# Optimization experiments

Measured on AMD Instinct MI355X. Metric: run time of the kernel, lower is better.

## Reference

```python
import jax, jax.numpy as jnp
import numpy as np

# Module constants (match init_kwargs)
H = 16            # num_heads
K = 64            # max_kernel_size
MAX_FREQ = 16.0
MIN_FREQ = 1.0
HALF_S = 16       # int(32**(1/1)) // 2
S = 2 * HALF_S + 1  # 33 sample offsets: -16..16
MAX_RECEPTIVE = HALF_S * MAX_FREQ  # 256.0


def setup_inputs() -> dict:
    key = jax.random.key(0)
    ks = jax.random.split(key, 6)
    B, L, C = 1, 4096, 1024
    x = jax.random.normal(ks[0], (B, L, C), dtype=jnp.float32)
    # Learned params (random small scale so offsets/kernels vary; torch inits
    # wave_proj to zeros but that degenerates the math under test).
    Ww = jax.random.normal(ks[1], (2 * H, C), dtype=jnp.float32) * 0.02
    bw = jnp.zeros((2 * H,), dtype=jnp.float32)
    Wk = jax.random.normal(ks[2], (H * K, C), dtype=jnp.float32) * 0.02
    bk = jnp.zeros((H * K,), dtype=jnp.float32)
    Wo = jax.random.normal(ks[3], (C, C), dtype=jnp.float32) * 0.02
    return {"x": x, "Ww": Ww, "bw": bw, "Wk": Wk, "bk": bk, "Wo": Wo}


def reference(x, Ww, bw, Wk, bk, Wo):
    B, L, C = x.shape
    D = C // H
    dt = x.dtype
    grid = jnp.arange(-HALF_S, HALF_S + 1, dtype=dt)  # (S,)

    # Predict per-position frequency / phase (averaged over heads)
    wp = jax.nn.silu(x @ Ww.T + bw).reshape(B, L, 2, H)
    freq = jax.nn.sigmoid(wp[:, :, 0]) * (MAX_FREQ - MIN_FREQ) + MIN_FREQ  # (B,L,H)
    phase = jnp.tanh(wp[:, :, 1]) * MAX_FREQ
    freq_avg = freq.mean(-1)    # (B,L)
    phase_avg = phase.mean(-1)  # (B,L)

    # Sample positions & gather indices
    rel_pos = grid[None, None, :] * freq_avg[..., None] + phase_avg[..., None]  # (B,L,S)
    centers = jnp.arange(L, dtype=dt)
    sample_pos = centers[None, :, None] + rel_pos                               # (B,L,S)
    valid = (sample_pos >= 0) & (sample_pos < L)
    sample_idx = jnp.clip(sample_pos.astype(jnp.int32), 0, L - 1)               # trunc toward 0, like torch .long()

    # Gather values: (B,L,S,C) -> (B,L,H,S,D)
    values = jax.vmap(lambda xf, idx: xf[idx])(x, sample_idx)
    values = values.reshape(B, L, S, H, D).transpose(0, 1, 3, 2, 4)

    # Kernel profile, linearly interpolated to sample positions
    kernel_max = jax.nn.silu(x @ Wk.T + bk).reshape(B, L, H, K)
    norm_pos = jnp.clip((rel_pos + MAX_RECEPTIVE) / (2.0 * MAX_RECEPTIVE), 0.0, 1.0)
    idx_float = norm_pos * (K - 1)                       # (B,L,S)
    idx_floor = jnp.clip(idx_float.astype(jnp.int32), 0, K - 2)
    w_ceil = (idx_float - idx_floor.astype(dt))[:, :, None, :]  # (B,L,1,S)
    w_floor = 1.0 - w_ceil
    ifl = jnp.broadcast_to(idx_floor[:, :, None, :], (B, L, H, S))
    k_floor = jnp.take_along_axis(kernel_max, ifl, axis=-1)
    k_ceil = jnp.take_along_axis(kernel_max, ifl + 1, axis=-1)
    kernel = (k_floor * w_floor + k_ceil * w_ceil) * valid[:, :, None, :].astype(dt)
    kernel = kernel / (kernel.sum(-1, keepdims=True) + 1e-8)

    out = jnp.einsum('blhsd,blhs->blhd', values, kernel).reshape(B, L, C)
    out = jax.nn.silu(out @ Wo.T)
    return out
```

## Files before the change

kernel.cpp:

```cpp
#include <hip/hip_runtime.h>
#include <math.h>

#define LDIM 4096
#define CDIM 1024
#define HDIM 16
#define KDIM 64
#define SDIM 33
#define HALF_SS 16
#define MAXF 16.0f
#define MINF 1.0f
#define MAXR 256.0f

typedef double d4 __attribute__((ext_vector_type(4)));

#define MFMA_F64 __builtin_amdgcn_mfma_f64_16x16x4f64

__device__ __forceinline__ float sigmoid_np(float z) {
  float e = (float)exp(-(double)z);
  return __fdiv_rn(1.0f, __fadd_rn(1.0f, e));
}
__device__ __forceinline__ float silu_f(float z) {
  return __fmul_rn(z, sigmoid_np(z));
}

__device__ __forceinline__ float np_pairwise_sum(const float* a, int n) {
  float r[8];
#pragma unroll
  for (int j = 0; j < 8; ++j) r[j] = a[j];
  int i = 8;
  for (; i + 8 <= n; i += 8)
#pragma unroll
    for (int j = 0; j < 8; ++j) r[j] = __fadd_rn(r[j], a[i + j]);
  float res = __fadd_rn(__fadd_rn(__fadd_rn(r[0], r[1]), __fadd_rn(r[2], r[3])),
                        __fadd_rn(__fadd_rn(r[4], r[5]), __fadd_rn(r[6], r[7])));
  for (; i < n; ++i) res = __fadd_rn(res, a[i]);
  return res;
}

__global__ __launch_bounds__(256) void wave_kernel(
    const float* __restrict__ x, const float* __restrict__ Ww,
    const float* __restrict__ bw, float* __restrict__ fa, float* __restrict__ pa) {
  __shared__ float xs[CDIM];
  __shared__ float wp[2 * HDIM];
  int l = blockIdx.x;
  int tid = threadIdx.x;
  const float* xrow = x + (size_t)l * CDIM;
  for (int c = tid; c < CDIM; c += 256) xs[c] = xrow[c];
  __syncthreads();
  int j = tid >> 3, sub = tid & 7;
  const float* wrow = Ww + j * CDIM;
  double acc = 0.0;
  for (int c = sub; c < CDIM; c += 8) acc += (double)xs[c] * (double)wrow[c];
  for (int off = 4; off; off >>= 1) acc += __shfl_down(acc, off, 8);
  if (sub == 0) {
    float v32 = (float)(acc + (double)bw[j]);
    wp[j] = silu_f(v32);
  }
  __syncthreads();
  if (tid == 0) {
    float fv[HDIM], pv[HDIM];
    for (int h = 0; h < HDIM; ++h) {
      fv[h] = __fadd_rn(__fmul_rn(sigmoid_np(wp[h]), MAXF - MINF), MINF);
      float t32 = (float)tanh((double)wp[HDIM + h]);
      pv[h] = __fmul_rn(t32, MAXF);
    }
    fa[l] = __fdiv_rn(np_pairwise_sum(fv, HDIM), (float)HDIM);
    pa[l] = __fdiv_rn(np_pairwise_sum(pv, HDIM), (float)HDIM);
  }
}

__global__ __launch_bounds__(256) void gemm_bt_silu_f64(
    const float* __restrict__ A, const float* __restrict__ B,
    const float* __restrict__ bias, float* __restrict__ Cout,
    int M, int N, int Kd) {
  __shared__ float Asf[128][36];
  __shared__ float Bsf[64][36];
  int tid = threadIdx.x;
  int w  = tid >> 6;
  int l  = tid & 63;
  int m0 = blockIdx.y * 128, n0 = blockIdx.x * 64;

  d4 zv = (d4)(0.0);
  double lane_d = (double)l;
  d4 pA = MFMA_F64(lane_d, 1.0, zv, 0, 0, 0);
  d4 pB = MFMA_F64(1.0, lane_d, zv, 0, 0, 0);
  int sa0 = (int)pA[0], sb0 = (int)pB[0];
  bool aH1 = ((sa0 & 3) == 0);
  bool bH1 = ((sb0 & 3) == 0);
  int lmA = aH1 ? (l & 15) : (l >> 2);
  int lqA = aH1 ? (l >> 4) : (l & 3);
  int lmB = bH1 ? (l & 15) : (l >> 2);
  int lqB = bH1 ? (l >> 4) : (l & 3);
  int di[4], dj[4];
#pragma unroll
  for (int r = 0; r < 4; ++r) {
    int va = (int)pA[r], vb = (int)pB[r];
    di[r] = (aH1 ? ((va - 96) >> 2) : ((va - 6) >> 4)) & 15;
    dj[r] = (bH1 ? ((vb - 96) >> 2) : ((vb - 6) >> 4)) & 15;
  }

  d4 acc[8];
#pragma unroll
  for (int i = 0; i < 8; ++i) acc[i] = (d4)(0.0);

  for (int kt = 0; kt < Kd; kt += 32) {
#pragma unroll
    for (int qi = 0; qi < 4; ++qi) {
      int e = tid + 256 * qi;
      int row = e >> 3, j = e & 7;
      float4 v = *(const float4*)(A + (size_t)(m0 + row) * Kd + kt + 4 * j);
      Asf[row][j] = v.x; Asf[row][j + 8] = v.y;
      Asf[row][j + 16] = v.z; Asf[row][j + 24] = v.w;
    }
#pragma unroll
    for (int qi = 0; qi < 2; ++qi) {
      int e = tid + 256 * qi;
      int row = e >> 3, j = e & 7;
      float4 v = *(const float4*)(B + (size_t)(n0 + row) * Kd + kt + 4 * j);
      Bsf[row][j] = v.x; Bsf[row][j + 8] = v.y;
      Bsf[row][j + 16] = v.z; Bsf[row][j + 24] = v.w;
    }
    __syncthreads();
#pragma unroll
    for (int t = 0; t < 2; ++t) {
      float4 bv = *(const float4*)&Bsf[16 * w + lmB][8 * lqB + 4 * t];
      float4 av0 = *(const float4*)&Asf[lmA][8 * lqA + 4 * t];
      float4 av1 = *(const float4*)&Asf[16 + lmA][8 * lqA + 4 * t];
      float4 av2 = *(const float4*)&Asf[32 + lmA][8 * lqA + 4 * t];
      float4 av3 = *(const float4*)&Asf[48 + lmA][8 * lqA + 4 * t];
      float4 av4 = *(const float4*)&Asf[64 + lmA][8 * lqA + 4 * t];
      float4 av5 = *(const float4*)&Asf[80 + lmA][8 * lqA + 4 * t];
      float4 av6 = *(const float4*)&Asf[96 + lmA][8 * lqA + 4 * t];
      float4 av7 = *(const float4*)&Asf[112 + lmA][8 * lqA + 4 * t];
      float bs[4] = {bv.x, bv.y, bv.z, bv.w};
      float as0[4] = {av0.x, av0.y, av0.z, av0.w};
      float as1[4] = {av1.x, av1.y, av1.z, av1.w};
      float as2[4] = {av2.x, av2.y, av2.z, av2.w};
      float as3[4] = {av3.x, av3.y, av3.z, av3.w};
      float as4[4] = {av4.x, av4.y, av4.z, av4.w};
      float as5[4] = {av5.x, av5.y, av5.z, av5.w};
      float as6[4] = {av6.x, av6.y, av6.z, av6.w};
      float as7[4] = {av7.x, av7.y, av7.z, av7.w};
#pragma unroll
      for (int s = 0; s < 4; ++s) {
        double bd = (double)bs[s];
        acc[0] = MFMA_F64((double)as0[s], bd, acc[0], 0, 0, 0);
        acc[1] = MFMA_F64((double)as1[s], bd, acc[1], 0, 0, 0);
        acc[2] = MFMA_F64((double)as2[s], bd, acc[2], 0, 0, 0);
        acc[3] = MFMA_F64((double)as3[s], bd, acc[3], 0, 0, 0);
        acc[4] = MFMA_F64((double)as4[s], bd, acc[4], 0, 0, 0);
        acc[5] = MFMA_F64((double)as5[s], bd, acc[5], 0, 0, 0);
        acc[6] = MFMA_F64((double)as6[s], bd, acc[6], 0, 0, 0);
        acc[7] = MFMA_F64((double)as7[s], bd, acc[7], 0, 0, 0);
      }
    }
    __syncthreads();
  }

#pragma unroll
  for (int mt = 0; mt < 8; ++mt) {
#pragma unroll
    for (int r = 0; r < 4; ++r) {
      int mm = m0 + 16 * mt + di[r];
      int nn = n0 + 16 * w + dj[r];
      float v32 = (float)acc[mt][r];
      v32 = __fadd_rn(v32, bias[nn]);
      Cout[(size_t)mm * N + nn] = silu_f(v32);
    }
  }
}

__global__ __launch_bounds__(256) void gemm_bt_silu_f32(
    const float* __restrict__ A, const float* __restrict__ B,
    float* __restrict__ Cout, int M, int N, int Kd) {
  __shared__ float Asf[16][128];
  __shared__ float Bsf[16][128];
  int tid = threadIdx.x;
  int tx = tid & 15, ty = tid >> 4;
  int m0 = blockIdx.y * 128, n0 = blockIdx.x * 128;
  float acc[8][8] = {};
  for (int kt = 0; kt < Kd; kt += 16) {
#pragma unroll
    for (int q = 0; q < 2; ++q) {
      int e = tid + 256 * q;
      int row = e >> 2, kq = (e & 3) * 4;
      float4 va = *(const float4*)(A + (size_t)(m0 + row) * Kd + kt + kq);
      Asf[kq + 0][row] = va.x; Asf[kq + 1][row] = va.y;
      Asf[kq + 2][row] = va.z; Asf[kq + 3][row] = va.w;
      float4 vb = *(const float4*)(B + (size_t)(n0 + row) * Kd + kt + kq);
      Bsf[kq + 0][row] = vb.x; Bsf[kq + 1][row] = vb.y;
      Bsf[kq + 2][row] = vb.z; Bsf[kq + 3][row] = vb.w;
    }
    __syncthreads();
#pragma unroll
    for (int kk = 0; kk < 16; ++kk) {
      float4 a0 = *(const float4*)&Asf[kk][ty * 8];
      float4 a1 = *(const float4*)&Asf[kk][ty * 8 + 4];
      float4 b0 = *(const float4*)&Bsf[kk][tx * 8];
      float4 b1 = *(const float4*)&Bsf[kk][tx * 8 + 4];
      float a[8] = {a0.x, a0.y, a0.z, a0.w, a1.x, a1.y, a1.z, a1.w};
      float b[8] = {b0.x, b0.y, b0.z, b0.w, b1.x, b1.y, b1.z, b1.w};
#pragma unroll
      for (int i = 0; i < 8; ++i)
#pragma unroll
        for (int j2 = 0; j2 < 8; ++j2) acc[i][j2] += a[i] * b[j2];
    }
    __syncthreads();
  }
#pragma unroll
  for (int i = 0; i < 8; ++i) {
    int mm = m0 + ty * 8 + i;
#pragma unroll
    for (int j2 = 0; j2 < 8; ++j2) {
      int nn = n0 + tx * 8 + j2;
      Cout[(size_t)mm * N + nn] = silu_f(acc[i][j2]);
    }
  }
}

__global__ __launch_bounds__(256) void conv_kernel(
    const float* __restrict__ x, const float* __restrict__ km,
    const float* __restrict__ fa, const float* __restrict__ pa,
    float* __restrict__ conv) {
  int l = blockIdx.x;
  int tid = threadIdx.x;
  __shared__ int s_idx[SDIM];
  __shared__ int s_ifl[SDIM];
  __shared__ float s_wc[SDIM];
  __shared__ float s_val[SDIM];
  __shared__ float kern[HDIM][SDIM];
  __shared__ float s_den[HDIM];
  if (tid < SDIM) {
    float f = fa[l], p = pa[l];
    float rel = __fadd_rn(__fmul_rn((float)(tid - HALF_SS), f), p);
    float pos = __fadd_rn((float)l, rel);
    bool valid = (pos >= 0.f) && (pos < (float)LDIM);
    int idx = (int)pos;
    idx = min(max(idx, 0), LDIM - 1);
    s_idx[tid] = idx;
    s_val[tid] = valid ? 1.f : 0.f;
    float np_ = __fdiv_rn(__fadd_rn(rel, MAXR), 2.f * MAXR);
    np_ = fminf(fmaxf(np_, 0.f), 1.f);
    float idxf = __fmul_rn(np_, (float)(KDIM - 1));
    int ifl = (int)idxf;
    ifl = min(max(ifl, 0), KDIM - 2);
    s_ifl[tid] = ifl;
    s_wc[tid] = __fsub_rn(idxf, (float)ifl);
  }
  __syncthreads();
  for (int t = tid; t < HDIM * SDIM; t += 256) {
    int h = t / SDIM, s = t - h * SDIM;
    const float* kb = km + (size_t)l * CDIM + h * KDIM;
    float wc = s_wc[s];
    float wf = __fsub_rn(1.f, wc);
    float v = __fadd_rn(__fmul_rn(kb[s_ifl[s]], wf), __fmul_rn(kb[s_ifl[s] + 1], wc));
    kern[h][s] = __fmul_rn(v, s_val[s]);
  }
  __syncthreads();
  if (tid < HDIM) {
    float sum = np_pairwise_sum(&kern[tid][0], SDIM);
    s_den[tid] = __fadd_rn(sum, 1e-8f);
  }
  __syncthreads();
  for (int t = tid; t < HDIM * SDIM; t += 256) {
    int h = t / SDIM, s = t - h * SDIM;
    kern[h][s] = __fdiv_rn(kern[h][s], s_den[h]);
  }
  __syncthreads();
  float acc[4] = {0.f, 0.f, 0.f, 0.f};
  for (int s = 0; s < SDIM; ++s) {
    const float* xr = x + (size_t)s_idx[s] * CDIM;
#pragma unroll
    for (int q = 0; q < 4; ++q) {
      int c = tid + q * 256;
      acc[q] = __fadd_rn(acc[q], __fmul_rn(xr[c], kern[c >> 6][s]));
    }
  }
#pragma unroll
  for (int q = 0; q < 4; ++q) {
    int c = tid + q * 256;
    conv[(size_t)l * CDIM + c] = acc[q];
  }
}

extern "C" void kernel_launch(void* const* d_in, const int* in_sizes, int n_in,
                              void* d_out, int out_size, void* d_ws, size_t ws_size,
                              hipStream_t stream) {
  const float* x  = (const float*)d_in[0];
  const float* Ww = (const float*)d_in[1];
  const float* bw = (const float*)d_in[2];
  const float* Wk = (const float*)d_in[3];
  const float* bk = (const float*)d_in[4];
  const float* Wo = (const float*)d_in[5];
  float* out = (float*)d_out;

  float* fa   = (float*)d_ws;
  float* pa   = fa + LDIM;
  float* km   = pa + LDIM;
  float* conv = km + (size_t)LDIM * CDIM;

  wave_kernel<<<LDIM, 256, 0, stream>>>(x, Ww, bw, fa, pa);

  dim3 kmgrid(CDIM / 64, LDIM / 128);
  gemm_bt_silu_f64<<<kmgrid, 256, 0, stream>>>(x, Wk, bk, km, LDIM, CDIM, CDIM);

  conv_kernel<<<LDIM, 256, 0, stream>>>(x, km, fa, pa, conv);

  dim3 ogrid(CDIM / 128, LDIM / 128);
  gemm_bt_silu_f32<<<ogrid, 256, 0, stream>>>(conv, Wo, out, LDIM, CDIM, CDIM);
}
```

Baseline: 456.1 us.

## Double-buffer f64 MFMA GEMM tiles and retile output GEMM to 512 threads

The f64-MFMA GEMM that produces the kernel profile now uses two shared-memory buffers, so global loads for the next K tile are issued before the current tile's MFMAs and written to the other buffer afterwards. This hides global load latency and removes one barrier per iteration, at the cost of doubled LDS and more live registers. The output GEMM moves from 256 to 512 threads, each computing a 4x8 micro-tile, with padded LDS rows and float4 stores. This trades more threads per block for fewer accumulators per thread.

```diff
diff --git a/kernel.cpp b/kernel.cpp
--- a/kernel.cpp
+++ b/kernel.cpp
@@ -73,8 +73,8 @@
     const float* __restrict__ A, const float* __restrict__ B,
     const float* __restrict__ bias, float* __restrict__ Cout,
     int M, int N, int Kd) {
-  __shared__ float Asf[128][36];
-  __shared__ float Bsf[64][36];
+  __shared__ float Asf[2][128][36];
+  __shared__ float Bsf[2][64][36];
   int tid = threadIdx.x;
   int w  = tid >> 6;
   int l  = tid & 63;
@@ -103,35 +103,59 @@
 #pragma unroll
   for (int i = 0; i < 8; ++i) acc[i] = (d4)(0.0);
 
-  for (int kt = 0; kt < Kd; kt += 32) {
-#pragma unroll
-    for (int qi = 0; qi < 4; ++qi) {
-      int e = tid + 256 * qi;
-      int row = e >> 3, j = e & 7;
-      float4 v = *(const float4*)(A + (size_t)(m0 + row) * Kd + kt + 4 * j);
-      Asf[row][j] = v.x; Asf[row][j + 8] = v.y;
-      Asf[row][j + 16] = v.z; Asf[row][j + 24] = v.w;
-    }
-#pragma unroll
-    for (int qi = 0; qi < 2; ++qi) {
-      int e = tid + 256 * qi;
-      int row = e >> 3, j = e & 7;
-      float4 v = *(const float4*)(B + (size_t)(n0 + row) * Kd + kt + 4 * j);
-      Bsf[row][j] = v.x; Bsf[row][j + 8] = v.y;
-      Bsf[row][j + 16] = v.z; Bsf[row][j + 24] = v.w;
-    }
-    __syncthreads();
+  int rA = tid >> 3, jc = tid & 7;
+  const float* Agp = A + (size_t)(m0 + rA) * Kd + 4 * jc;
+  const float* Bgp = B + (size_t)(n0 + rA) * Kd + 4 * jc;
+
+  {
+    float4 a0 = *(const float4*)(Agp);
+    float4 a1 = *(const float4*)(Agp + (size_t)32 * Kd);
+    float4 a2 = *(const float4*)(Agp + (size_t)64 * Kd);
+    float4 a3 = *(const float4*)(Agp + (size_t)96 * Kd);
+    float4 b0 = *(const float4*)(Bgp);
+    float4 b1 = *(const float4*)(Bgp + (size_t)32 * Kd);
+    Asf[0][rA +  0][jc] = a0.x; Asf[0][rA +  0][jc + 8] = a0.y;
+    Asf[0][rA +  0][jc + 16] = a0.z; Asf[0][rA +  0][jc + 24] = a0.w;
+    Asf[0][rA + 32][jc] = a1.x; Asf[0][rA + 32][jc + 8] = a1.y;
+    Asf[0][rA + 32][jc + 16] = a1.z; Asf[0][rA + 32][jc + 24] = a1.w;
+    Asf[0][rA + 64][jc] = a2.x; Asf[0][rA + 64][jc + 8] = a2.y;
+    Asf[0][rA + 64][jc + 16] = a2.z; Asf[0][rA + 64][jc + 24] = a2.w;
+    Asf[0][rA + 96][jc] = a3.x; Asf[0][rA + 96][jc + 8] = a3.y;
+    Asf[0][rA + 96][jc + 16] = a3.z; Asf[0][rA + 96][jc + 24] = a3.w;
+    Bsf[0][rA +  0][jc] = b0.x; Bsf[0][rA +  0][jc + 8] = b0.y;
+    Bsf[0][rA +  0][jc + 16] = b0.z; Bsf[0][rA +  0][jc + 24] = b0.w;
+    Bsf[0][rA + 32][jc] = b1.x; Bsf[0][rA + 32][jc + 8] = b1.y;
+    Bsf[0][rA + 32][jc + 16] = b1.z; Bsf[0][rA + 32][jc + 24] = b1.w;
+  }
+  __syncthreads();
+
+  const int NT = Kd >> 5;
+  int cur = 0;
+  for (int tt = 0; tt < NT; ++tt) {
+    float4 qa0, qa1, qa2, qa3, qb0, qb1;
+    bool pf = (tt + 1 < NT);
+    if (pf) {
+      int ko = (tt + 1) * 32;
+      qa0 = *(const float4*)(Agp + ko);
+      qa1 = *(const float4*)(Agp + (size_t)32 * Kd + ko);
+      qa2 = *(const float4*)(Agp + (size_t)64 * Kd + ko);
+      qa3 = *(const float4*)(Agp + (size_t)96 * Kd + ko);
+      qb0 = *(const float4*)(Bgp + ko);
+      qb1 = *(const float4*)(Bgp + (size_t)32 * Kd + ko);
+    }
+    const float (*As)[36] = Asf[cur];
+    const float (*Bs)[36] = Bsf[cur];
 #pragma unroll
     for (int t = 0; t < 2; ++t) {
-      float4 bv = *(const float4*)&Bsf[16 * w + lmB][8 * lqB + 4 * t];
-      float4 av0 = *(const float4*)&Asf[lmA][8 * lqA + 4 * t];
-      float4 av1 = *(const float4*)&Asf[16 + lmA][8 * lqA + 4 * t];
-      float4 av2 = *(const float4*)&Asf[32 + lmA][8 * lqA + 4 * t];
-      float4 av3 = *(const float4*)&Asf[48 + lmA][8 * lqA + 4 * t];
-      float4 av4 = *(const float4*)&Asf[64 + lmA][8 * lqA + 4 * t];
-      float4 av5 = *(const float4*)&Asf[80 + lmA][8 * lqA + 4 * t];
-      float4 av6 = *(const float4*)&Asf[96 + lmA][8 * lqA + 4 * t];
-      float4 av7 = *(const float4*)&Asf[112 + lmA][8 * lqA + 4 * t];
+      float4 bv = *(const float4*)&Bs[16 * w + lmB][8 * lqB + 4 * t];
+      float4 av0 = *(const float4*)&As[lmA][8 * lqA + 4 * t];
+      float4 av1 = *(const float4*)&As[16 + lmA][8 * lqA + 4 * t];
+      float4 av2 = *(const float4*)&As[32 + lmA][8 * lqA + 4 * t];
+      float4 av3 = *(const float4*)&As[48 + lmA][8 * lqA + 4 * t];
+      float4 av4 = *(const float4*)&As[64 + lmA][8 * lqA + 4 * t];
+      float4 av5 = *(const float4*)&As[80 + lmA][8 * lqA + 4 * t];
+      float4 av6 = *(const float4*)&As[96 + lmA][8 * lqA + 4 * t];
+      float4 av7 = *(const float4*)&As[112 + lmA][8 * lqA + 4 * t];
       float bs[4] = {bv.x, bv.y, bv.z, bv.w};
       float as0[4] = {av0.x, av0.y, av0.z, av0.w};
       float as1[4] = {av1.x, av1.y, av1.z, av1.w};
@@ -154,7 +178,24 @@
         acc[7] = MFMA_F64((double)as7[s], bd, acc[7], 0, 0, 0);
       }
     }
+    if (pf) {
+      float (*Ad)[36] = Asf[cur ^ 1];
+      float (*Bd)[36] = Bsf[cur ^ 1];
+      Ad[rA +  0][jc] = qa0.x; Ad[rA +  0][jc + 8] = qa0.y;
+      Ad[rA +  0][jc + 16] = qa0.z; Ad[rA +  0][jc + 24] = qa0.w;
+      Ad[rA + 32][jc] = qa1.x; Ad[rA + 32][jc + 8] = qa1.y;
+      Ad[rA + 32][jc + 16] = qa1.z; Ad[rA + 32][jc + 24] = qa1.w;
+      Ad[rA + 64][jc] = qa2.x; Ad[rA + 64][jc + 8] = qa2.y;
+      Ad[rA + 64][jc + 16] = qa2.z; Ad[rA + 64][jc + 24] = qa2.w;
+      Ad[rA + 96][jc] = qa3.x; Ad[rA + 96][jc + 8] = qa3.y;
+      Ad[rA + 96][jc + 16] = qa3.z; Ad[rA + 96][jc + 24] = qa3.w;
+      Bd[rA +  0][jc] = qb0.x; Bd[rA +  0][jc + 8] = qb0.y;
+      Bd[rA +  0][jc + 16] = qb0.z; Bd[rA +  0][jc + 24] = qb0.w;
+      Bd[rA + 32][jc] = qb1.x; Bd[rA + 32][jc + 8] = qb1.y;
+      Bd[rA + 32][jc + 16] = qb1.z; Bd[rA + 32][jc + 24] = qb1.w;
+    }
     __syncthreads();
+    cur ^= 1;
   }
 
 #pragma unroll
@@ -170,51 +211,51 @@
   }
 }
 
-__global__ __launch_bounds__(256) void gemm_bt_silu_f32(
+__global__ __launch_bounds__(512) void gemm_bt_silu_f32(
     const float* __restrict__ A, const float* __restrict__ B,
     float* __restrict__ Cout, int M, int N, int Kd) {
-  __shared__ float Asf[16][128];
-  __shared__ float Bsf[16][128];
+  __shared__ float Asf[16][132];
+  __shared__ float Bsf[16][132];
   int tid = threadIdx.x;
-  int tx = tid & 15, ty = tid >> 4;
+  int tx = tid & 15;
+  int ty = tid >> 4;
   int m0 = blockIdx.y * 128, n0 = blockIdx.x * 128;
-  float acc[8][8] = {};
+  float acc[4][8] = {};
+  int rS = tid >> 2, kq = (tid & 3) * 4;
   for (int kt = 0; kt < Kd; kt += 16) {
-#pragma unroll
-    for (int q = 0; q < 2; ++q) {
-      int e = tid + 256 * q;
-      int row = e >> 2, kq = (e & 3) * 4;
-      float4 va = *(const float4*)(A + (size_t)(m0 + row) * Kd + kt + kq);
-      Asf[kq + 0][row] = va.x; Asf[kq + 1][row] = va.y;
-      Asf[kq + 2][row] = va.z; Asf[kq + 3][row] = va.w;
-      float4 vb = *(const float4*)(B + (size_t)(n0 + row) * Kd + kt + kq);
-      Bsf[kq + 0][row] = vb.x; Bsf[kq + 1][row] = vb.y;
-      Bsf[kq + 2][row] = vb.z; Bsf[kq + 3][row] = vb.w;
+    {
+      float4 va = *(const float4*)(A + (size_t)(m0 + rS) * Kd + kt + kq);
+      Asf[kq + 0][rS] = va.x; Asf[kq + 1][rS] = va.y;
+      Asf[kq + 2][rS] = va.z; Asf[kq + 3][rS] = va.w;
+      float4 vb = *(const float4*)(B + (size_t)(n0 + rS) * Kd + kt + kq);
+      Bsf[kq + 0][rS] = vb.x; Bsf[kq + 1][rS] = vb.y;
+      Bsf[kq + 2][rS] = vb.z; Bsf[kq + 3][rS] = vb.w;
     }
     __syncthreads();
 #pragma unroll
     for (int kk = 0; kk < 16; ++kk) {
-      float4 a0 = *(const float4*)&Asf[kk][ty * 8];
-      float4 a1 = *(const float4*)&Asf[kk][ty * 8 + 4];
-      float4 b0 = *(const float4*)&Bsf[kk][tx * 8];
-      float4 b1 = *(const float4*)&Bsf[kk][tx * 8 + 4];
-      float a[8] = {a0.x, a0.y, a0.z, a0.w, a1.x, a1.y, a1.z, a1.w};
+      float4 a0 = *(const float4*)&Asf[kk][ty * 4];
+      float4 b0 = *(const float4*)&Bsf[kk][tx * 4];
+      float4 b1 = *(const float4*)&Bsf[kk][tx * 4 + 64];
+      float a[4] = {a0.x, a0.y, a0.z, a0.w};
       float b[8] = {b0.x, b0.y, b0.z, b0.w, b1.x, b1.y, b1.z, b1.w};
 #pragma unroll
-      for (int i = 0; i < 8; ++i)
+      for (int i = 0; i < 4; ++i)
 #pragma unroll
         for (int j2 = 0; j2 < 8; ++j2) acc[i][j2] += a[i] * b[j2];
     }
     __syncthreads();
   }
 #pragma unroll
-  for (int i = 0; i < 8; ++i) {
-    int mm = m0 + ty * 8 + i;
-#pragma unroll
-    for (int j2 = 0; j2 < 8; ++j2) {
-      int nn = n0 + tx * 8 + j2;
-      Cout[(size_t)mm * N + nn] = silu_f(acc[i][j2]);
-    }
+  for (int i = 0; i < 4; ++i) {
+    int mm = m0 + ty * 4 + i;
+    float4 o0, o1;
+    o0.x = silu_f(acc[i][0]); o0.y = silu_f(acc[i][1]);
+    o0.z = silu_f(acc[i][2]); o0.w = silu_f(acc[i][3]);
+    o1.x = silu_f(acc[i][4]); o1.y = silu_f(acc[i][5]);
+    o1.z = silu_f(acc[i][6]); o1.w = silu_f(acc[i][7]);
+    *(float4*)&Cout[(size_t)mm * N + n0 + 4 * tx] = o0;
+    *(float4*)&Cout[(size_t)mm * N + n0 + 64 + 4 * tx] = o1;
   }
 }
 
@@ -307,5 +348,5 @@
   conv_kernel<<<LDIM, 256, 0, stream>>>(x, km, fa, pa, conv);
 
   dim3 ogrid(CDIM / 128, LDIM / 128);
-  gemm_bt_silu_f32<<<ogrid, 256, 0, stream>>>(conv, Wo, out, LDIM, CDIM, CDIM);
-}
+  gemm_bt_silu_f32<<<ogrid, 512, 0, stream>>>(conv, Wo, out, LDIM, CDIM, CDIM);
+}
```

New measurement: 458.7 us. Within noise of the previous version (+0.6%).
